# Optimization experiments

Measured on AMD Instinct MI355X. Metric: run time of the kernel, lower is better.

## Reference

```python
import jax, jax.numpy as jnp
import numpy as np

B, S, R, C_Q, C_KV, H, C_A = 1, 128, 256, 256, 256, 8, 32


def setup_inputs() -> dict:
    key = jax.random.key(0)
    ks = jax.random.split(key, 11)
    scale = 0.02
    q = jax.random.normal(ks[0], (B, S, R, C_Q), jnp.float32)
    kv = jax.random.normal(ks[1], (B, S, R, C_KV), jnp.float32)
    bias = jax.random.normal(ks[2], (B, 1, R, R, H), jnp.float32)
    bias_mask = jax.random.randint(ks[3], (B, S, R), 0, 2).astype(jnp.float32)
    w_q = jax.random.normal(ks[4], (C_Q, H, C_A), jnp.float32) * scale
    w_k = jax.random.normal(ks[5], (C_KV, H, C_A), jnp.float32) * scale
    w_v = jax.random.normal(ks[6], (C_KV, H, C_A), jnp.float32) * scale
    w_g = jax.random.normal(ks[7], (C_Q, H, C_A), jnp.float32) * scale
    b_g = jax.random.normal(ks[8], (H, C_A), jnp.float32) * scale
    w_o = jax.random.normal(ks[9], (H, C_A, C_Q), jnp.float32) * scale
    b_o = jax.random.normal(ks[10], (C_Q,), jnp.float32) * scale
    return {"q": q, "kv": kv, "bias": bias, "bias_mask": bias_mask,
            "w_q": w_q, "w_k": w_k, "w_v": w_v, "w_g": w_g, "b_g": b_g,
            "w_o": w_o, "b_o": b_o}


def reference(q, kv, bias, bias_mask, w_q, w_k, w_v, w_g, b_g, w_o, b_o):
    # q, kv: [B, S, R, C]; attention over residue dim R within each row s.
    c_a = w_q.shape[-1]
    normsize = 1.0 / jnp.sqrt(jnp.asarray(c_a, q.dtype))
    Q = jnp.einsum('bsqc,chd->bsqhd', q, w_q) * normsize  # [B,S,R,H,Ca]
    K = jnp.einsum('bskc,chd->bskhd', kv, w_k)
    V = jnp.einsum('bskc,chd->bskhd', kv, w_v)
    # affinity: [B,S,Q,K,H]
    AT = jnp.einsum('bsqhd,bskhd->bsqkh', Q, K)
    mask_bias = (bias_mask[:, :, None, :, None] - 1.0) * 1e9  # [B,S,1,K,1]
    AT = AT + bias + mask_bias
    AT = jax.nn.softmax(AT, axis=-2)  # softmax over K
    O = jnp.einsum('bsqkh,bskhd->bsqhd', AT, V)
    G = jax.nn.sigmoid(jnp.einsum('bsqc,chd->bsqhd', q, w_g) + b_g)
    O = O * G
    out = jnp.einsum('bsqhd,hdc->bsqc', O, w_o) + b_o  # [B,S,R,C_Q]
    return out
```

## Files before the change

kernel.cpp:

```cpp
#include <hip/hip_runtime.h>

typedef __bf16 bf16;
typedef __bf16 bf16x8 __attribute__((ext_vector_type(8)));
typedef __bf16 bf16x4 __attribute__((ext_vector_type(4)));
typedef float  f32x4  __attribute__((ext_vector_type(4)));
typedef unsigned int u32;
typedef unsigned int u32x2 __attribute__((ext_vector_type(2)));
typedef unsigned int u32x4 __attribute__((ext_vector_type(4)));
typedef unsigned short u16;

#define MFMA16(a, b, c) __builtin_amdgcn_mfma_f32_16x16x32_bf16((a), (b), (c), 0, 0, 0)
#define L2E 1.4426950408889634f


typedef __attribute__((address_space(3))) u32 lds_u32;
typedef const __attribute__((address_space(1))) u32 glob_u32;
__device__ __forceinline__ void gll16(const void* g, void* l) {
    __builtin_amdgcn_global_load_lds((glob_u32*)g, (lds_u32*)l, 16, 0, 0);
}

__device__ __forceinline__ u32 pk2(float lo, float hi) {
    u16 a = __builtin_bit_cast(u16, (bf16)lo);
    u16 b = __builtin_bit_cast(u16, (bf16)hi);
    return ((u32)b << 16) | (u32)a;
}

__device__ __forceinline__ float fexp2(float x) {
#if __has_builtin(__builtin_amdgcn_exp2f)
    return __builtin_amdgcn_exp2f(x);
#else
    return exp2f(x);
#endif
}
__device__ __forceinline__ float frcp(float x) {
#if __has_builtin(__builtin_amdgcn_rcpf)
    return __builtin_amdgcn_rcpf(x);
#else
    return 1.0f / x;
#endif
}

__global__ __launch_bounds__(256) void prep_kernel(
    const float* __restrict__ bias,
    const float* __restrict__ w_q, const float* __restrict__ w_k,
    const float* __restrict__ w_v, const float* __restrict__ w_g,
    const float* __restrict__ w_o, const float* __restrict__ b_g,
    float* __restrict__ biasT,
    bf16* __restrict__ Wqg, bf16* __restrict__ Wkv, bf16* __restrict__ Wo,
    float* __restrict__ b_gL)
{
    const float norm = 0.17677669529663687f * L2E;
    const int gid = blockIdx.x * 256 + threadIdx.x;
    const int gsz = gridDim.x * 256;

    for (int u = gid; u < 524288; u += gsz) {
        int h = u >> 16, qq = (u >> 8) & 255, kk = u & 255;
        biasT[u] = bias[(((qq << 8) + kk) << 3) + h] * L2E;
    }
    for (int u = gid; u < 131072; u += gsz) {
        int n = u >> 8, k = u & 255;
        float v = (n < 256) ? w_q[k * 256 + n] * norm : w_g[k * 256 + (n - 256)] * L2E;
        Wqg[u] = (bf16)v;
    }
    for (int u = gid; u < 131072; u += gsz) {
        int n = u >> 8, k = u & 255;
        float v = (n < 256) ? w_k[k * 256 + n] : w_v[k * 256 + (n - 256)];
        Wkv[u] = (bf16)v;
    }
    for (int u = gid; u < 65536; u += gsz) {
        int n = u >> 8, k = u & 255;
        Wo[u] = (bf16)w_o[k * 256 + n];
    }
    for (int u = gid; u < 256; u += gsz) b_gL[u] = b_g[u] * L2E;
}

template<int AMODE, bool F32OUT>
__device__ __forceinline__ void gemm_core(
    const void* __restrict__ Ap, const bf16* __restrict__ Bw,
    bf16* __restrict__ Cb, float* __restrict__ Cf, const float* __restrict__ bo,
    int m0, int n0, int ntot)
{
    __shared__ __align__(16) bf16 As[128 * 32];
    __shared__ __align__(16) bf16 Bs[128 * 32];

    const bf16*  A16 = (const bf16*)Ap;
    const float* A32 = (const float*)Ap;

    const int tid  = threadIdx.x;
    const int lane = tid & 63, wave = tid >> 6;
    const int quad = lane >> 4, lc = lane & 15;
    const int wr = wave >> 1, wc = wave & 1;

    const int r0 = tid >> 2, p0 = tid & 3;
    const size_t offA0 = (size_t)(m0 + r0) * 256 + p0 * 8;
    const size_t offA1 = (size_t)(m0 + 64 + r0) * 256 + p0 * 8;
    const bf16* gB0 = Bw + (size_t)(n0 + r0) * 256 + p0 * 8;
    const bf16* gB1 = Bw + (size_t)(n0 + 64 + r0) * 256 + p0 * 8;
    bf16* lA0 = As + tid * 8;
    bf16* lA1 = As + (tid + 256) * 8;
    bf16* lB0 = Bs + tid * 8;
    bf16* lB1 = Bs + (tid + 256) * 8;

    f32x4 acc[4][4];
    #pragma unroll
    for (int i = 0; i < 4; ++i)
        #pragma unroll
        for (int j = 0; j < 4; ++j) acc[i][j] = f32x4{0.f, 0.f, 0.f, 0.f};

    #pragma unroll 1
    for (int kb = 0; kb < 8; ++kb) {
        const int ko = kb * 32;
        if constexpr (AMODE == 0) {
            gll16(A16 + offA0 + ko, lA0);
            gll16(A16 + offA1 + ko, lA1);
            gll16(gB0 + ko, lB0);
            gll16(gB1 + ko, lB1);
        } else {
            float4 x0 = *(const float4*)(A32 + offA0 + ko);
            float4 x1 = *(const float4*)(A32 + offA0 + ko + 4);
            float4 y0 = *(const float4*)(A32 + offA1 + ko);
            float4 y1 = *(const float4*)(A32 + offA1 + ko + 4);
            gll16(gB0 + ko, lB0);
            gll16(gB1 + ko, lB1);
            bf16x8 ta, tb;
            ta[0]=(bf16)x0.x; ta[1]=(bf16)x0.y; ta[2]=(bf16)x0.z; ta[3]=(bf16)x0.w;
            ta[4]=(bf16)x1.x; ta[5]=(bf16)x1.y; ta[6]=(bf16)x1.z; ta[7]=(bf16)x1.w;
            tb[0]=(bf16)y0.x; tb[1]=(bf16)y0.y; tb[2]=(bf16)y0.z; tb[3]=(bf16)y0.w;
            tb[4]=(bf16)y1.x; tb[5]=(bf16)y1.y; tb[6]=(bf16)y1.z; tb[7]=(bf16)y1.w;
            *(bf16x8*)lA0 = ta;
            *(bf16x8*)lA1 = tb;
        }
        __syncthreads();

        bf16x8 aF[4], bF[4];
        #pragma unroll
        for (int mt = 0; mt < 4; ++mt)
            aF[mt] = *(const bf16x8*)(As + (wr * 64 + mt * 16 + lc) * 32 + quad * 8);
        #pragma unroll
        for (int nt = 0; nt < 4; ++nt)
            bF[nt] = *(const bf16x8*)(Bs + (wc * 64 + nt * 16 + lc) * 32 + quad * 8);
        #pragma unroll
        for (int mt = 0; mt < 4; ++mt)
            #pragma unroll
            for (int nt = 0; nt < 4; ++nt)
                acc[mt][nt] = MFMA16(aF[mt], bF[nt], acc[mt][nt]);
        __syncthreads();
    }

    #pragma unroll
    for (int mt = 0; mt < 4; ++mt) {
        #pragma unroll
        for (int nt = 0; nt < 4; ++nt) {
            const int row = m0 + wr * 64 + mt * 16 + quad * 4;
            const int col = n0 + wc * 64 + nt * 16 + lc;
            if (F32OUT) {
                float b = bo[col];
                #pragma unroll
                for (int rr = 0; rr < 4; ++rr)
                    Cf[(size_t)(row + rr) * ntot + col] = acc[mt][nt][rr] + b;
            } else {
                #pragma unroll
                for (int rr = 0; rr < 4; ++rr)
                    Cb[(size_t)(row + rr) * ntot + col] = (bf16)acc[mt][nt][rr];
            }
        }
    }
}

__global__ __launch_bounds__(256) void proj_kernel(
    const float* __restrict__ qf, const float* __restrict__ kvf,
    const bf16* __restrict__ Wqg, const bf16* __restrict__ Wkv,
    bf16* __restrict__ QG, bf16* __restrict__ KV)
{
    int bid = blockIdx.x;
    bool sel = bid >= 1024;
    int b = sel ? bid - 1024 : bid;
    int m0 = (b & 255) * 128, n0 = (b >> 8) * 128;
    gemm_core<1, false>(sel ? kvf : qf, sel ? Wkv : Wqg,
                        sel ? KV : QG, nullptr, nullptr, m0, n0, 512);
}

__global__ __launch_bounds__(256) void outproj_kernel(
    const bf16* __restrict__ OG, const bf16* __restrict__ Wo,
    const float* __restrict__ bo, float* __restrict__ out)
{
    int b = blockIdx.x;
    int m0 = (b & 255) * 128, n0 = (b >> 8) * 128;
    gemm_core<0, true>(OG, Wo, nullptr, out, bo, m0, n0, 256);
}

#define A_OFF_MASK 0
#define A_OFF_K    1024
#define A_OFF_VT   21504
#define A_LDS_TOT  (21504 + 32 * 264 * 2)

__global__ __launch_bounds__(256) void attn_kernel(
    const bf16* __restrict__ QG, const bf16* __restrict__ KV,
    const float* __restrict__ biasT, const float* __restrict__ bias_mask,
    const float* __restrict__ b_gL, bf16* __restrict__ OG)
{
    __shared__ __align__(16) char smem[A_LDS_TOT];
    float* maskadd = (float*)(smem + A_OFF_MASK);
    bf16*  Ks      = (bf16*)(smem + A_OFF_K);
    bf16*  Vt      = (bf16*)(smem + A_OFF_VT);

    const int tid  = threadIdx.x;
    const int wave = tid >> 6, lane = tid & 63;
    const int quad = lane >> 4, lc = lane & 15;
    const int h = blockIdx.x >> 7;
    const int s = blockIdx.x & 127;

    maskadd[tid] = (bias_mask[s * 256 + tid] - 1.0f) * (1e9f * L2E);
    {
        const bf16* kvrow = KV + (size_t)(s * 256 + tid) * 512 + h * 32;
        #pragma unroll
        for (int j = 0; j < 4; ++j)
            *(bf16x8*)(Ks + tid * 40 + j * 8) = *(const bf16x8*)(kvrow + j * 8);
        bf16x8 vx[4];
        #pragma unroll
        for (int j = 0; j < 4; ++j) vx[j] = *(const bf16x8*)(kvrow + 256 + j * 8);
        #pragma unroll
        for (int d = 0; d < 32; ++d)
            Vt[d * 264 + tid] = vx[d >> 3][d & 7];
    }
    __syncthreads();

    const f32x4 bg0 = *(const f32x4*)(b_gL + h * 32 + quad * 4);
    const f32x4 bg1 = *(const f32x4*)(b_gL + h * 32 + 16 + quad * 4);

    #pragma unroll 1
    for (int p = 0; p < 4; ++p) {
        const int q0 = (wave * 4 + p) * 16;

        bf16x8 qf = *(const bf16x8*)(QG + (size_t)(s * 256 + q0 + lc) * 512 + h * 32 + quad * 8);

        const float* bT = biasT + (((size_t)h * 256 + q0 + lc) << 8) + quad * 4;
        u32x2 cw[16];
        float sum = 0.f;
        #pragma unroll
        for (int half = 0; half < 2; ++half) {
            f32x4 sc[8];
            #pragma unroll
            for (int k8 = 0; k8 < 8; ++k8) {
                const int kt = half * 8 + k8;
                bf16x8 kf = *(const bf16x8*)(Ks + (kt * 16 + lc) * 40 + quad * 8);
                f32x4 z = {0.f, 0.f, 0.f, 0.f};
                sc[k8] = MFMA16(kf, qf, z);
            }
            #pragma unroll
            for (int k8 = 0; k8 < 8; ++k8) {
                const int kt = half * 8 + k8;
                f32x4 bv = *(const f32x4*)(bT + kt * 16);
                f32x4 mv = *(const f32x4*)(maskadd + kt * 16 + quad * 4);
                f32x4 t = sc[k8] + bv + mv;
                float e0 = fexp2(t[0]);
                float e1 = fexp2(t[1]);
                float e2 = fexp2(t[2]);
                float e3 = fexp2(t[3]);
                sum += (e0 + e1) + (e2 + e3);
                cw[kt] = u32x2{pk2(e0, e1), pk2(e2, e3)};
            }
            __builtin_amdgcn_sched_barrier(0x6);
        }

        const bf16* gp = QG + (size_t)(s * 256 + q0 + lc) * 512 + 256 + h * 32 + quad * 4;
        bf16x4 gv0 = *(const bf16x4*)(gp);
        bf16x4 gv1 = *(const bf16x4*)(gp + 16);

        f32x4 o0 = {0.f, 0.f, 0.f, 0.f}, o1 = {0.f, 0.f, 0.f, 0.f};
        #pragma unroll
        for (int ks = 0; ks < 8; ++ks) {
            u32 c0 = cw[2 * ks].x,     c1 = cw[2 * ks].y;
            u32 c2 = cw[2 * ks + 1].x, c3 = cw[2 * ks + 1].y;
            u32x2 s02 = __builtin_amdgcn_permlane32_swap(c0, c2, false, false);
            u32x2 s13 = __builtin_amdgcn_permlane32_swap(c1, c3, false, false);
            u32x2 e02 = __builtin_amdgcn_permlane16_swap(s02.x, s02.y, false, false);
            u32x2 e13 = __builtin_amdgcn_permlane16_swap(s13.x, s13.y, false, false);
            u32x4 pw = {e02.x, e13.x, e02.y, e13.y};
            bf16x8 pf = __builtin_bit_cast(bf16x8, pw);
            bf16x8 v0 = *(const bf16x8*)(Vt + lc * 264 + ks * 32 + quad * 8);
            bf16x8 v1 = *(const bf16x8*)(Vt + (16 + lc) * 264 + ks * 32 + quad * 8);
            o0 = MFMA16(v0, pf, o0);
            o1 = MFMA16(v1, pf, o1);
        }

        sum += __shfl_xor(sum, 16, 64);
        sum += __shfl_xor(sum, 32, 64);
        const float inv = frcp(sum);

        bf16* op = OG + (size_t)(s * 256 + q0 + lc) * 256 + h * 32 + quad * 4;
        #pragma unroll
        for (int nt = 0; nt < 2; ++nt) {
            f32x4 ov = nt ? o1 : o0;
            f32x4 bg = nt ? bg1 : bg0;
            bf16x4 gv = nt ? gv1 : gv0;
            bf16x4 ob;
            #pragma unroll
            for (int rr = 0; rr < 4; ++rr) {
                float e = fexp2(-((float)gv[rr] + bg[rr]));
                float g = frcp(1.0f + e);
                ob[rr] = (bf16)(ov[rr] * (inv * g));
            }
            *(bf16x4*)(op + nt * 16) = ob;
        }
    }
}

extern "C" void kernel_launch(void* const* d_in, const int* in_sizes, int n_in,
                              void* d_out, int out_size, void* d_ws, size_t ws_size,
                              hipStream_t stream)
{
    (void)in_sizes; (void)n_in; (void)out_size; (void)ws_size;
    const float* q    = (const float*)d_in[0];
    const float* kv   = (const float*)d_in[1];
    const float* bias = (const float*)d_in[2];
    const float* mask = (const float*)d_in[3];
    const float* w_q  = (const float*)d_in[4];
    const float* w_k  = (const float*)d_in[5];
    const float* w_v  = (const float*)d_in[6];
    const float* w_g  = (const float*)d_in[7];
    const float* b_g  = (const float*)d_in[8];
    const float* w_o  = (const float*)d_in[9];
    const float* b_o  = (const float*)d_in[10];
    float* out = (float*)d_out;

    char* ws = (char*)d_ws;
    bf16*  OG    = (bf16*)(ws + 0);
    bf16*  QG    = (bf16*)(ws + 33554432);
    bf16*  KV    = (bf16*)(ws + 67108864);
    float* biasT = (float*)(ws + 100663296);
    bf16*  Wqg   = (bf16*)(ws + 102760448);
    bf16*  Wkv   = (bf16*)(ws + 103022592);
    bf16*  Wo    = (bf16*)(ws + 103284736);
    float* b_gL  = (float*)(ws + 103415808);

    prep_kernel<<<256, 256, 0, stream>>>(bias, w_q, w_k, w_v, w_g, w_o, b_g,
                                         biasT, Wqg, Wkv, Wo, b_gL);
    proj_kernel<<<2048, 256, 0, stream>>>(q, kv, Wqg, Wkv, QG, KV);
    attn_kernel<<<1024, 256, 0, stream>>>(QG, KV, biasT, mask, b_gL, OG);
    outproj_kernel<<<512, 256, 0, stream>>>(OG, Wo, b_o, out);
}
```

Before: 213.0 us.

## Double-buffer LDS tiles in GEMM core to overlap loads with MFMA

Adds a second LDS buffer for the A and B tiles of the shared GEMM routine and prefetches the next K-slice while MFMAs run on the current one, cutting one barrier per iteration. For the fp32 A path, the global loads are issued before compute and converted to bf16 and stored to LDS afterwards. The aim is to hide global-load latency behind matrix math. The cost is doubled LDS use (32KB per block) and more live registers, which may lower occupancy.

```diff
diff --git a/kernel.cpp b/kernel.cpp
--- a/kernel.cpp
+++ b/kernel.cpp
@@ -25,6 +25,13 @@
     return ((u32)b << 16) | (u32)a;
 }
 
+__device__ __forceinline__ bf16x8 cvt8(float4 a, float4 b) {
+    bf16x8 t;
+    t[0]=(bf16)a.x; t[1]=(bf16)a.y; t[2]=(bf16)a.z; t[3]=(bf16)a.w;
+    t[4]=(bf16)b.x; t[5]=(bf16)b.y; t[6]=(bf16)b.z; t[7]=(bf16)b.w;
+    return t;
+}
+
 __device__ __forceinline__ float fexp2(float x) {
 #if __has_builtin(__builtin_amdgcn_exp2f)
     return __builtin_amdgcn_exp2f(x);
@@ -80,8 +87,8 @@
     bf16* __restrict__ Cb, float* __restrict__ Cf, const float* __restrict__ bo,
     int m0, int n0, int ntot)
 {
-    __shared__ __align__(16) bf16 As[128 * 32];
-    __shared__ __align__(16) bf16 Bs[128 * 32];
+    __shared__ __align__(16) bf16 As[2][128 * 32];
+    __shared__ __align__(16) bf16 Bs[2][128 * 32];
 
     const bf16*  A16 = (const bf16*)Ap;
     const float* A32 = (const float*)Ap;
@@ -96,10 +103,6 @@
     const size_t offA1 = (size_t)(m0 + 64 + r0) * 256 + p0 * 8;
     const bf16* gB0 = Bw + (size_t)(n0 + r0) * 256 + p0 * 8;
     const bf16* gB1 = Bw + (size_t)(n0 + 64 + r0) * 256 + p0 * 8;
-    bf16* lA0 = As + tid * 8;
-    bf16* lA1 = As + (tid + 256) * 8;
-    bf16* lB0 = Bs + tid * 8;
-    bf16* lB1 = Bs + (tid + 256) * 8;
 
     f32x4 acc[4][4];
     #pragma unroll
@@ -107,43 +110,64 @@
         #pragma unroll
         for (int j = 0; j < 4; ++j) acc[i][j] = f32x4{0.f, 0.f, 0.f, 0.f};
 
+    if constexpr (AMODE == 0) {
+        gll16(A16 + offA0, As[0] + tid * 8);
+        gll16(A16 + offA1, As[0] + (tid + 256) * 8);
+    } else {
+        float4 x0 = *(const float4*)(A32 + offA0);
+        float4 x1 = *(const float4*)(A32 + offA0 + 4);
+        float4 y0 = *(const float4*)(A32 + offA1);
+        float4 y1 = *(const float4*)(A32 + offA1 + 4);
+        *(bf16x8*)(As[0] + tid * 8)         = cvt8(x0, x1);
+        *(bf16x8*)(As[0] + (tid + 256) * 8) = cvt8(y0, y1);
+    }
+    gll16(gB0, Bs[0] + tid * 8);
+    gll16(gB1, Bs[0] + (tid + 256) * 8);
+    __syncthreads();
+
     #pragma unroll 1
     for (int kb = 0; kb < 8; ++kb) {
-        const int ko = kb * 32;
-        if constexpr (AMODE == 0) {
-            gll16(A16 + offA0 + ko, lA0);
-            gll16(A16 + offA1 + ko, lA1);
-            gll16(gB0 + ko, lB0);
-            gll16(gB1 + ko, lB1);
-        } else {
-            float4 x0 = *(const float4*)(A32 + offA0 + ko);
-            float4 x1 = *(const float4*)(A32 + offA0 + ko + 4);
-            float4 y0 = *(const float4*)(A32 + offA1 + ko);
-            float4 y1 = *(const float4*)(A32 + offA1 + ko + 4);
-            gll16(gB0 + ko, lB0);
-            gll16(gB1 + ko, lB1);
-            bf16x8 ta, tb;
-            ta[0]=(bf16)x0.x; ta[1]=(bf16)x0.y; ta[2]=(bf16)x0.z; ta[3]=(bf16)x0.w;
-            ta[4]=(bf16)x1.x; ta[5]=(bf16)x1.y; ta[6]=(bf16)x1.z; ta[7]=(bf16)x1.w;
-            tb[0]=(bf16)y0.x; tb[1]=(bf16)y0.y; tb[2]=(bf16)y0.z; tb[3]=(bf16)y0.w;
-            tb[4]=(bf16)y1.x; tb[5]=(bf16)y1.y; tb[6]=(bf16)y1.z; tb[7]=(bf16)y1.w;
-            *(bf16x8*)lA0 = ta;
-            *(bf16x8*)lA1 = tb;
-        }
-        __syncthreads();
+        bf16* Ac = As[kb & 1];
+        bf16* Bc = Bs[kb & 1];
+        bf16* An = As[(kb & 1) ^ 1];
+        bf16* Bn = Bs[(kb & 1) ^ 1];
+        const int kn = (kb + 1) * 32;
+        const bool pf = kb < 7;
+
+        float4 x0, x1, y0, y1;
+        if (pf) {
+            if constexpr (AMODE == 0) {
+                gll16(A16 + offA0 + kn, An + tid * 8);
+                gll16(A16 + offA1 + kn, An + (tid + 256) * 8);
+            } else {
+                x0 = *(const float4*)(A32 + offA0 + kn);
+                x1 = *(const float4*)(A32 + offA0 + kn + 4);
+                y0 = *(const float4*)(A32 + offA1 + kn);
+                y1 = *(const float4*)(A32 + offA1 + kn + 4);
+            }
+            gll16(gB0 + kn, Bn + tid * 8);
+            gll16(gB1 + kn, Bn + (tid + 256) * 8);
+        }
 
         bf16x8 aF[4], bF[4];
         #pragma unroll
         for (int mt = 0; mt < 4; ++mt)
-            aF[mt] = *(const bf16x8*)(As + (wr * 64 + mt * 16 + lc) * 32 + quad * 8);
+            aF[mt] = *(const bf16x8*)(Ac + (wr * 64 + mt * 16 + lc) * 32 + quad * 8);
         #pragma unroll
         for (int nt = 0; nt < 4; ++nt)
-            bF[nt] = *(const bf16x8*)(Bs + (wc * 64 + nt * 16 + lc) * 32 + quad * 8);
+            bF[nt] = *(const bf16x8*)(Bc + (wc * 64 + nt * 16 + lc) * 32 + quad * 8);
         #pragma unroll
         for (int mt = 0; mt < 4; ++mt)
             #pragma unroll
             for (int nt = 0; nt < 4; ++nt)
                 acc[mt][nt] = MFMA16(aF[mt], bF[nt], acc[mt][nt]);
+
+        if (pf) {
+            if constexpr (AMODE == 1) {
+                *(bf16x8*)(An + tid * 8)         = cvt8(x0, x1);
+                *(bf16x8*)(An + (tid + 256) * 8) = cvt8(y0, y1);
+            }
+        }
         __syncthreads();
     }
 
```

Result: no change. 216.3 us (+1.5%).

## Replace LDS-staged GEMM with register-direct 32x32 MFMA projection GEMMs

Applied to the files above, without the earlier changes.

The projection and output GEMMs no longer stage A and B tiles through shared memory with barriers. Each wave now loads its operand fragments straight from global memory into registers and issues 32x32x16 bf16 MFMAs on four accumulators. This removes LDS traffic and the two __syncthreads per k-step. In exchange, operands are no longer reused across waves in the block, so global/L2 load traffic rises, and the loads are less coalesced (each lane reads 16-32 bytes from a different row).

```diff
diff --git a/kernel.cpp b/kernel.cpp
--- a/kernel.cpp
+++ b/kernel.cpp
@@ -4,25 +4,28 @@
 typedef __bf16 bf16x8 __attribute__((ext_vector_type(8)));
 typedef __bf16 bf16x4 __attribute__((ext_vector_type(4)));
 typedef float  f32x4  __attribute__((ext_vector_type(4)));
+typedef float  f32x16 __attribute__((ext_vector_type(16)));
 typedef unsigned int u32;
 typedef unsigned int u32x2 __attribute__((ext_vector_type(2)));
 typedef unsigned int u32x4 __attribute__((ext_vector_type(4)));
 typedef unsigned short u16;
 
 #define MFMA16(a, b, c) __builtin_amdgcn_mfma_f32_16x16x32_bf16((a), (b), (c), 0, 0, 0)
+#define MFMA32(a, b, c) __builtin_amdgcn_mfma_f32_32x32x16_bf16((a), (b), (c), 0, 0, 0)
 #define L2E 1.4426950408889634f
 
-
-typedef __attribute__((address_space(3))) u32 lds_u32;
-typedef const __attribute__((address_space(1))) u32 glob_u32;
-__device__ __forceinline__ void gll16(const void* g, void* l) {
-    __builtin_amdgcn_global_load_lds((glob_u32*)g, (lds_u32*)l, 16, 0, 0);
-}
 
 __device__ __forceinline__ u32 pk2(float lo, float hi) {
     u16 a = __builtin_bit_cast(u16, (bf16)lo);
     u16 b = __builtin_bit_cast(u16, (bf16)hi);
     return ((u32)b << 16) | (u32)a;
+}
+
+__device__ __forceinline__ bf16x8 cvt8(float4 a, float4 b) {
+    bf16x8 t;
+    t[0]=(bf16)a.x; t[1]=(bf16)a.y; t[2]=(bf16)a.z; t[3]=(bf16)a.w;
+    t[4]=(bf16)b.x; t[5]=(bf16)b.y; t[6]=(bf16)b.z; t[7]=(bf16)b.w;
+    return t;
 }
 
 __device__ __forceinline__ float fexp2(float x) {
@@ -75,93 +78,64 @@
 }
 
 template<int AMODE, bool F32OUT>
-__device__ __forceinline__ void gemm_core(
+__device__ __forceinline__ void sgemm_core(
     const void* __restrict__ Ap, const bf16* __restrict__ Bw,
     bf16* __restrict__ Cb, float* __restrict__ Cf, const float* __restrict__ bo,
     int m0, int n0, int ntot)
 {
-    __shared__ __align__(16) bf16 As[128 * 32];
-    __shared__ __align__(16) bf16 Bs[128 * 32];
-
+    const float* A32 = (const float*)Ap;
     const bf16*  A16 = (const bf16*)Ap;
-    const float* A32 = (const float*)Ap;
-
-    const int tid  = threadIdx.x;
-    const int lane = tid & 63, wave = tid >> 6;
-    const int quad = lane >> 4, lc = lane & 15;
+
+    const int lane = threadIdx.x & 63, wave = threadIdx.x >> 6;
+    const int l31 = lane & 31, hi = lane >> 5;
     const int wr = wave >> 1, wc = wave & 1;
-
-    const int r0 = tid >> 2, p0 = tid & 3;
-    const size_t offA0 = (size_t)(m0 + r0) * 256 + p0 * 8;
-    const size_t offA1 = (size_t)(m0 + 64 + r0) * 256 + p0 * 8;
-    const bf16* gB0 = Bw + (size_t)(n0 + r0) * 256 + p0 * 8;
-    const bf16* gB1 = Bw + (size_t)(n0 + 64 + r0) * 256 + p0 * 8;
-    bf16* lA0 = As + tid * 8;
-    bf16* lA1 = As + (tid + 256) * 8;
-    bf16* lB0 = Bs + tid * 8;
-    bf16* lB1 = Bs + (tid + 256) * 8;
-
-    f32x4 acc[4][4];
+    const int mbase = m0 + wr * 64;
+    const int nbase = n0 + wc * 64;
+
+    const size_t a0off = (size_t)(mbase + l31) * 256 + hi * 8;
+    const size_t a1off = a0off + 32 * 256;
+    const bf16* b0p = Bw + (size_t)(nbase + l31) * 256 + hi * 8;
+    const bf16* b1p = b0p + 32 * 256;
+
+    f32x16 acc00, acc01, acc10, acc11;
     #pragma unroll
-    for (int i = 0; i < 4; ++i)
-        #pragma unroll
-        for (int j = 0; j < 4; ++j) acc[i][j] = f32x4{0.f, 0.f, 0.f, 0.f};
-
-    #pragma unroll 1
-    for (int kb = 0; kb < 8; ++kb) {
-        const int ko = kb * 32;
-        if constexpr (AMODE == 0) {
-            gll16(A16 + offA0 + ko, lA0);
-            gll16(A16 + offA1 + ko, lA1);
-            gll16(gB0 + ko, lB0);
-            gll16(gB1 + ko, lB1);
+    for (int i = 0; i < 16; ++i) { acc00[i]=0.f; acc01[i]=0.f; acc10[i]=0.f; acc11[i]=0.f; }
+
+    #pragma unroll 2
+    for (int kb = 0; kb < 16; ++kb) {
+        const int k = kb * 16;
+        bf16x8 a0, a1;
+        if constexpr (AMODE == 1) {
+            float4 x0 = *(const float4*)(A32 + a0off + k);
+            float4 x1 = *(const float4*)(A32 + a0off + k + 4);
+            float4 y0 = *(const float4*)(A32 + a1off + k);
+            float4 y1 = *(const float4*)(A32 + a1off + k + 4);
+            a0 = cvt8(x0, x1);
+            a1 = cvt8(y0, y1);
         } else {
-            float4 x0 = *(const float4*)(A32 + offA0 + ko);
-            float4 x1 = *(const float4*)(A32 + offA0 + ko + 4);
-            float4 y0 = *(const float4*)(A32 + offA1 + ko);
-            float4 y1 = *(const float4*)(A32 + offA1 + ko + 4);
-            gll16(gB0 + ko, lB0);
-            gll16(gB1 + ko, lB1);
-            bf16x8 ta, tb;
-            ta[0]=(bf16)x0.x; ta[1]=(bf16)x0.y; ta[2]=(bf16)x0.z; ta[3]=(bf16)x0.w;
-            ta[4]=(bf16)x1.x; ta[5]=(bf16)x1.y; ta[6]=(bf16)x1.z; ta[7]=(bf16)x1.w;
-            tb[0]=(bf16)y0.x; tb[1]=(bf16)y0.y; tb[2]=(bf16)y0.z; tb[3]=(bf16)y0.w;
-            tb[4]=(bf16)y1.x; tb[5]=(bf16)y1.y; tb[6]=(bf16)y1.z; tb[7]=(bf16)y1.w;
-            *(bf16x8*)lA0 = ta;
-            *(bf16x8*)lA1 = tb;
-        }
-        __syncthreads();
-
-        bf16x8 aF[4], bF[4];
-        #pragma unroll
-        for (int mt = 0; mt < 4; ++mt)
-            aF[mt] = *(const bf16x8*)(As + (wr * 64 + mt * 16 + lc) * 32 + quad * 8);
-        #pragma unroll
-        for (int nt = 0; nt < 4; ++nt)
-            bF[nt] = *(const bf16x8*)(Bs + (wc * 64 + nt * 16 + lc) * 32 + quad * 8);
-        #pragma unroll
-        for (int mt = 0; mt < 4; ++mt)
+            a0 = *(const bf16x8*)(A16 + a0off + k);
+            a1 = *(const bf16x8*)(A16 + a1off + k);
+        }
+        bf16x8 b0 = *(const bf16x8*)(b0p + k);
+        bf16x8 b1 = *(const bf16x8*)(b1p + k);
+        acc00 = MFMA32(a0, b0, acc00);
+        acc01 = MFMA32(a0, b1, acc01);
+        acc10 = MFMA32(a1, b0, acc10);
+        acc11 = MFMA32(a1, b1, acc11);
+    }
+
+    #pragma unroll
+    for (int mt = 0; mt < 2; ++mt) {
+        #pragma unroll
+        for (int nt = 0; nt < 2; ++nt) {
+            const f32x16 v = mt ? (nt ? acc11 : acc10) : (nt ? acc01 : acc00);
+            const int col = nbase + nt * 32 + l31;
+            const float bb = F32OUT ? bo[col] : 0.f;
             #pragma unroll
-            for (int nt = 0; nt < 4; ++nt)
-                acc[mt][nt] = MFMA16(aF[mt], bF[nt], acc[mt][nt]);
-        __syncthreads();
-    }
-
-    #pragma unroll
-    for (int mt = 0; mt < 4; ++mt) {
-        #pragma unroll
-        for (int nt = 0; nt < 4; ++nt) {
-            const int row = m0 + wr * 64 + mt * 16 + quad * 4;
-            const int col = n0 + wc * 64 + nt * 16 + lc;
-            if (F32OUT) {
-                float b = bo[col];
-                #pragma unroll
-                for (int rr = 0; rr < 4; ++rr)
-                    Cf[(size_t)(row + rr) * ntot + col] = acc[mt][nt][rr] + b;
-            } else {
-                #pragma unroll
-                for (int rr = 0; rr < 4; ++rr)
-                    Cb[(size_t)(row + rr) * ntot + col] = (bf16)acc[mt][nt][rr];
+            for (int r = 0; r < 16; ++r) {
+                const int row = mbase + mt * 32 + (r & 3) + 8 * (r >> 2) + 4 * hi;
+                if (F32OUT) Cf[(size_t)row * ntot + col] = v[r] + bb;
+                else        Cb[(size_t)row * ntot + col] = (bf16)v[r];
             }
         }
     }
@@ -176,8 +150,8 @@
     bool sel = bid >= 1024;
     int b = sel ? bid - 1024 : bid;
     int m0 = (b & 255) * 128, n0 = (b >> 8) * 128;
-    gemm_core<1, false>(sel ? kvf : qf, sel ? Wkv : Wqg,
-                        sel ? KV : QG, nullptr, nullptr, m0, n0, 512);
+    sgemm_core<1, false>(sel ? kvf : qf, sel ? Wkv : Wqg,
+                         sel ? KV : QG, nullptr, nullptr, m0, n0, 512);
 }
 
 __global__ __launch_bounds__(256) void outproj_kernel(
@@ -186,7 +160,7 @@
 {
     int b = blockIdx.x;
     int m0 = (b & 255) * 128, n0 = (b >> 8) * 128;
-    gemm_core<0, true>(OG, Wo, nullptr, out, bo, m0, n0, 256);
+    sgemm_core<0, true>(OG, Wo, nullptr, out, bo, m0, n0, 256);
 }
 
 #define A_OFF_MASK 0
```

Result: slower. 279.6 us (+31.2%).
